# Kernel optimization log

Measured on AMD Instinct MI355X. Metric: run time of the kernel, lower is better.

The kernel has to match this reference:

```python
import jax, jax.numpy as jnp
import numpy as np


def setup_inputs() -> dict:
    key = jax.random.key(0)
    kL, kx = jax.random.split(key)
    N, D, K = 4096, 256, 8
    L = jax.random.normal(kL, (N, N), dtype=jnp.float32)
    x = jax.random.normal(kx, (N, D), dtype=jnp.float32)
    # Taylor-like decaying filter coefficients (fixed, non-trained in the original)
    coeffs = jnp.asarray([1.0, 0.9, 0.45, 0.15, 0.0375, 0.0075, 0.00125, 0.000179],
                         dtype=jnp.float32)
    return {"L": L, "x": x, "coeffs": coeffs}


def reference(L, x, coeffs):
    """filter = sum_i coeffs[i] * L^i ; out = filter @ x.

    Same math as torch.stack([c*L.matrix_power(i)]).sum(0) @ x, but the powers
    are built with a single running product instead of K independent
    matrix_power calls.
    """
    N = L.shape[0]
    K = coeffs.shape[0]
    P = jnp.eye(N, dtype=L.dtype)          # L^0
    filt = coeffs[0] * P
    for i in range(1, K):                   # small fixed polynomial order
        P = P @ L                            # L^i
        filt = filt + coeffs[i] * P
    return filt @ x                          # [N, D]
```

## Files before the change

kernel.cpp:

```cpp
#include <hip/hip_runtime.h>
#include <hip/hip_bf16.h>

#define NDIM 4096
#define DDIM 256
#define KORD 8

#define BM 128
#define BN 64
#define BK 32
#define SPLITK 4
#define KSLICE (NDIM / SPLITK)
#define NSTEP (KSLICE / BK)
#define ELEMS (NDIM * DDIM)

typedef __attribute__((ext_vector_type(8))) short bf16x8;
typedef __attribute__((ext_vector_type(4))) float f32x4;

__device__ __forceinline__ ushort f2bf(float v) {
    __hip_bfloat16 h = __float2bfloat16(v);
    return *reinterpret_cast<ushort*>(&h);
}
__device__ __forceinline__ float bf2f(ushort u) {
    __hip_bfloat16 h = *reinterpret_cast<__hip_bfloat16*>(&u);
    return __bfloat162float(h);
}
__device__ __forceinline__ void split2(float v, ushort& h, ushort& l) {
    h = f2bf(v);
    l = f2bf(v - bf2f(h));
}
__device__ __forceinline__ uint4 pack8(const ushort* s) {
    uint4 r;
    r.x = (uint)s[0] | ((uint)s[1] << 16);
    r.y = (uint)s[2] | ((uint)s[3] << 16);
    r.z = (uint)s[4] | ((uint)s[5] << 16);
    r.w = (uint)s[6] | ((uint)s[7] << 16);
    return r;
}

__global__ __launch_bounds__(256)
void split_L(const float* __restrict__ L, ushort* __restrict__ Lhi,
             ushort* __restrict__ Llo)
{
    const int e0 = (blockIdx.x * 256 + threadIdx.x) * 8;
    float4 a = *(const float4*)&L[e0];
    float4 b = *(const float4*)&L[e0 + 4];
    float v[8] = {a.x, a.y, a.z, a.w, b.x, b.y, b.z, b.w};
    ushort h[8], l[8];
#pragma unroll
    for (int j = 0; j < 8; ++j) split2(v[j], h[j], l[j]);
    *(uint4*)&Lhi[e0] = pack8(h);
    *(uint4*)&Llo[e0] = pack8(l);
}

__global__ __launch_bounds__(256)
void split_x(const float* __restrict__ x, const float* __restrict__ coeffs,
             ushort* __restrict__ yhiT, ushort* __restrict__ yloT)
{
    __shared__ float tile[64][65];
    const float c = coeffs[KORD - 1];
    const int m0 = blockIdx.x * 64, n0 = blockIdx.y * 64;
    const int t = threadIdx.x;
    const int ml = t >> 2, n4 = (t & 3) * 16;
#pragma unroll
    for (int j = 0; j < 4; ++j) {
        float4 v = *(const float4*)&x[(size_t)(m0 + ml) * DDIM + n0 + n4 + j * 4];
        tile[ml][n4 + j * 4 + 0] = c * v.x;
        tile[ml][n4 + j * 4 + 1] = c * v.y;
        tile[ml][n4 + j * 4 + 2] = c * v.z;
        tile[ml][n4 + j * 4 + 3] = c * v.w;
    }
    __syncthreads();
    const int nl = t >> 2, m16 = (t & 3) * 16;
    ushort h[16], l[16];
#pragma unroll
    for (int j = 0; j < 16; ++j) split2(tile[m16 + j][nl], h[j], l[j]);
    const size_t ob = (size_t)(n0 + nl) * NDIM + m0 + m16;
    *(uint4*)&yhiT[ob]     = pack8(h);
    *(uint4*)&yhiT[ob + 8] = pack8(h + 8);
    *(uint4*)&yloT[ob]     = pack8(l);
    *(uint4*)&yloT[ob + 8] = pack8(l + 8);
}

__global__ __launch_bounds__(256, 2)
void gemm_fused(const ushort* __restrict__ Lhi, const ushort* __restrict__ Llo,
                const ushort* __restrict__ yhiT, const ushort* __restrict__ yloT,
                float* __restrict__ P)
{
    __shared__ ushort lds[2][12288];

    const int bid  = blockIdx.x;
    const int xcd  = bid & 7;
    const int slot = bid >> 3;
    const int nt   = slot & 3;
    const int panel = xcd * 16 + (slot >> 2);
    const int mt = panel & 31;
    const int z  = panel >> 5;

    const int m0 = mt * BM, n0 = nt * BN;
    const int kb = z * KSLICE;

    const int t = threadIdx.x;
    const int lane = t & 63, wid = t >> 6;
    const int wr = wid >> 1, wc = wid & 1;

    const int srow = t >> 2;
    const int kswz = ((t & 3) ^ (srow & 3)) * 8;
    const ushort* aH0 = Lhi + (size_t)(m0 + srow) * NDIM + kb + kswz;
    const ushort* aH1 = aH0 + (size_t)64 * NDIM;
    const ushort* aL0 = Llo + (size_t)(m0 + srow) * NDIM + kb + kswz;
    const ushort* aL1 = aL0 + (size_t)64 * NDIM;
    const ushort* bH  = yhiT + (size_t)(n0 + srow) * NDIM + kb + kswz;
    const ushort* bL  = yloT + (size_t)(n0 + srow) * NDIM + kb + kswz;
    const int wb = wid * 512;

#define GLD(src, c, dstoff)                                                  \
    __builtin_amdgcn_global_load_lds(                                        \
        (const __attribute__((address_space(1))) uint*)(src),                \
        (__attribute__((address_space(3))) uint*)(&lds[c][dstoff]), 16, 0, 0)

    const int frow = lane & 15;
    const int fsw  = ((lane >> 4) ^ (frow & 3)) * 8;
    const int arB  = (wr * 64 + frow) * 32 + fsw;
    const int brB  = (wc * 32 + frow) * 32 + fsw;

    f32x4 acc[4][2];
#pragma unroll
    for (int i = 0; i < 4; ++i)
#pragma unroll
        for (int j = 0; j < 2; ++j) acc[i][j] = (f32x4){0.f, 0.f, 0.f, 0.f};

    {
        const int ko = 0;
        GLD(aH0 + ko, 0, wb);        GLD(aH1 + ko, 0, 2048 + wb);
        GLD(aL0 + ko, 0, 4096 + wb); GLD(aL1 + ko, 0, 6144 + wb);
        GLD(bH + ko, 0, 8192 + wb);  GLD(bL + ko, 0, 10240 + wb);
    }
    __syncthreads();

    int cur = 0;
    for (int step = 0; step < NSTEP; ++step) {
        if (step + 1 < NSTEP) {
            const int ko = (step + 1) * BK;
            const int c = cur ^ 1;
            GLD(aH0 + ko, c, wb);        GLD(aH1 + ko, c, 2048 + wb);
            GLD(aL0 + ko, c, 4096 + wb); GLD(aL1 + ko, c, 6144 + wb);
            GLD(bH + ko, c, 8192 + wb);  GLD(bL + ko, c, 10240 + wb);
        }

        bf16x8 ah[4], al[4], bh[2], blv[2];
#pragma unroll
        for (int i = 0; i < 4; ++i) {
            ah[i] = *(const bf16x8*)&lds[cur][arB + i * 512];
            al[i] = *(const bf16x8*)&lds[cur][arB + i * 512 + 4096];
        }
#pragma unroll
        for (int j = 0; j < 2; ++j) {
            bh[j]  = *(const bf16x8*)&lds[cur][8192 + brB + j * 512];
            blv[j] = *(const bf16x8*)&lds[cur][10240 + brB + j * 512];
        }
#pragma unroll
        for (int i = 0; i < 4; ++i)
#pragma unroll
            for (int j = 0; j < 2; ++j) {
                acc[i][j] = __builtin_amdgcn_mfma_f32_16x16x32_bf16(
                    ah[i], bh[j], acc[i][j], 0, 0, 0);
                acc[i][j] = __builtin_amdgcn_mfma_f32_16x16x32_bf16(
                    ah[i], blv[j], acc[i][j], 0, 0, 0);
                acc[i][j] = __builtin_amdgcn_mfma_f32_16x16x32_bf16(
                    al[i], bh[j], acc[i][j], 0, 0, 0);
            }
        __syncthreads();
        cur ^= 1;
    }
#undef GLD

    float* Pp = P + (size_t)z * ELEMS;
    const int crow = (lane >> 4) * 4;
    const int ccol = lane & 15;
#pragma unroll
    for (int i = 0; i < 4; ++i)
#pragma unroll
        for (int j = 0; j < 2; ++j)
#pragma unroll
            for (int r = 0; r < 4; ++r)
                Pp[(size_t)(m0 + wr * 64 + i * 16 + crow + r) * DDIM
                   + n0 + wc * 32 + j * 16 + ccol] = acc[i][j][r];
}

__global__ __launch_bounds__(256)
void combine(const float* __restrict__ P, const float* __restrict__ x,
             const float* __restrict__ coeffs, const int ci, const int last,
             ushort* __restrict__ yhiT, ushort* __restrict__ yloT,
             float* __restrict__ out)
{
    __shared__ float tile[64][65];
    const float c = coeffs[ci];
    const int m0 = blockIdx.x * 64, n0 = blockIdx.y * 64;
    const int t = threadIdx.x;
    const int ml = t >> 2, n4 = (t & 3) * 16;
    const size_t base = (size_t)(m0 + ml) * DDIM + n0 + n4;
    float acc[16];
#pragma unroll
    for (int j = 0; j < 4; ++j) {
        float4 v = *(const float4*)&x[base + j * 4];
        acc[j * 4 + 0] = c * v.x; acc[j * 4 + 1] = c * v.y;
        acc[j * 4 + 2] = c * v.z; acc[j * 4 + 3] = c * v.w;
    }
#pragma unroll
    for (int s = 0; s < SPLITK; ++s) {
        const float* Pp = P + (size_t)s * ELEMS;
#pragma unroll
        for (int j = 0; j < 4; ++j) {
            float4 v = *(const float4*)&Pp[base + j * 4];
            acc[j * 4 + 0] += v.x; acc[j * 4 + 1] += v.y;
            acc[j * 4 + 2] += v.z; acc[j * 4 + 3] += v.w;
        }
    }
    if (last) {
#pragma unroll
        for (int j = 0; j < 4; ++j) {
            float4 v;
            v.x = acc[j * 4 + 0]; v.y = acc[j * 4 + 1];
            v.z = acc[j * 4 + 2]; v.w = acc[j * 4 + 3];
            *(float4*)&out[base + j * 4] = v;
        }
        return;
    }
#pragma unroll
    for (int j = 0; j < 16; ++j) tile[ml][n4 + j] = acc[j];
    __syncthreads();
    const int nl = t >> 2, m16 = (t & 3) * 16;
    ushort h[16], l[16];
#pragma unroll
    for (int j = 0; j < 16; ++j) split2(tile[m16 + j][nl], h[j], l[j]);
    const size_t ob = (size_t)(n0 + nl) * NDIM + m0 + m16;
    *(uint4*)&yhiT[ob]     = pack8(h);
    *(uint4*)&yhiT[ob + 8] = pack8(h + 8);
    *(uint4*)&yloT[ob]     = pack8(l);
    *(uint4*)&yloT[ob + 8] = pack8(l + 8);
}

extern "C" void kernel_launch(void* const* d_in, const int* in_sizes, int n_in,
                              void* d_out, int out_size, void* d_ws, size_t ws_size,
                              hipStream_t stream)
{
    const float* L      = (const float*)d_in[0];
    const float* x      = (const float*)d_in[1];
    const float* coeffs = (const float*)d_in[2];
    float* out = (float*)d_out;

    char* w = (char*)d_ws;
    ushort* Lhi  = (ushort*)w;
    ushort* Llo  = (ushort*)(w + (size_t)NDIM * NDIM * 2);
    float*  Pp   = (float*)(w + (size_t)NDIM * NDIM * 4);
    ushort* yhiT = (ushort*)(w + (size_t)NDIM * NDIM * 4 + (size_t)SPLITK * ELEMS * 4);
    ushort* yloT = yhiT + (size_t)DDIM * NDIM;

    split_L<<<NDIM * NDIM / (256 * 8), 256, 0, stream>>>(L, Lhi, Llo);
    split_x<<<dim3(NDIM / 64, DDIM / 64), 256, 0, stream>>>(x, coeffs, yhiT, yloT);

    for (int i = KORD - 2; i >= 0; --i) {
        gemm_fused<<<SPLITK * 128, 256, 0, stream>>>(Lhi, Llo, yhiT, yloT, Pp);
        combine<<<dim3(NDIM / 64, DDIM / 64), 256, 0, stream>>>(
            Pp, x, coeffs, i, (i == 0) ? 1 : 0, yhiT, yloT, out);
    }
}
```

Baseline: 294.1 us.

## Widen GEMM tile to 128x128, deepen split-K and double-prefetch stages

The split-K GEMM tile grows from 128x64 to 128x128, so each block covers twice the output columns. This halves how many times the split L operand is re-read from memory. Split-K doubles to 8 to keep the same block count. The main loop now keeps two stages in flight, using explicit vmcnt waits and raw barriers in place of __syncthreads, and raises wave priority around the MFMA block. In exchange, the fp32 partial-sum buffer and the combine pass read twice as many partials, and the larger accumulator raises register pressure.

```diff
diff --git a/kernel.cpp b/kernel.cpp
--- a/kernel.cpp
+++ b/kernel.cpp
@@ -6,12 +6,14 @@
 #define KORD 8
 
 #define BM 128
-#define BN 64
+#define BN 128
 #define BK 32
-#define SPLITK 4
+#define SPLITK 8
 #define KSLICE (NDIM / SPLITK)
 #define NSTEP (KSLICE / BK)
 #define ELEMS (NDIM * DDIM)
+
+#define LBUF 16384
 
 typedef __attribute__((ext_vector_type(8))) short bf16x8;
 typedef __attribute__((ext_vector_type(4))) float f32x4;
@@ -86,15 +88,13 @@
                 const ushort* __restrict__ yhiT, const ushort* __restrict__ yloT,
                 float* __restrict__ P)
 {
-    __shared__ ushort lds[2][12288];
+    __shared__ ushort lds[2 * LBUF];
 
     const int bid  = blockIdx.x;
-    const int xcd  = bid & 7;
+    const int z    = bid & 7;
     const int slot = bid >> 3;
-    const int nt   = slot & 3;
-    const int panel = xcd * 16 + (slot >> 2);
-    const int mt = panel & 31;
-    const int z  = panel >> 5;
+    const int nt   = slot & 1;
+    const int mt   = slot >> 1;
 
     const int m0 = mt * BM, n0 = nt * BN;
     const int kb = z * KSLICE;
@@ -103,75 +103,90 @@
     const int lane = t & 63, wid = t >> 6;
     const int wr = wid >> 1, wc = wid & 1;
 
-    const int srow = t >> 2;
-    const int kswz = ((t & 3) ^ (srow & 3)) * 8;
-    const ushort* aH0 = Lhi + (size_t)(m0 + srow) * NDIM + kb + kswz;
-    const ushort* aH1 = aH0 + (size_t)64 * NDIM;
-    const ushort* aL0 = Llo + (size_t)(m0 + srow) * NDIM + kb + kswz;
-    const ushort* aL1 = aL0 + (size_t)64 * NDIM;
-    const ushort* bH  = yhiT + (size_t)(n0 + srow) * NDIM + kb + kswz;
-    const ushort* bL  = yloT + (size_t)(n0 + srow) * NDIM + kb + kswz;
+    const int rowS = t >> 2;
+    const int ksw  = ((t & 3) ^ (rowS & 3)) * 8;
+    const ushort* sAh = Lhi  + (size_t)(m0 + rowS) * NDIM + kb + ksw;
+    const ushort* sAl = Llo  + (size_t)(m0 + rowS) * NDIM + kb + ksw;
+    const ushort* sBh = yhiT + (size_t)(n0 + rowS) * NDIM + kb + ksw;
+    const ushort* sBl = yloT + (size_t)(n0 + rowS) * NDIM + kb + ksw;
+    const size_t R64 = (size_t)64 * NDIM;
     const int wb = wid * 512;
 
-#define GLD(src, c, dstoff)                                                  \
+#define GLD(src, dstoff)                                                     \
     __builtin_amdgcn_global_load_lds(                                        \
         (const __attribute__((address_space(1))) uint*)(src),                \
-        (__attribute__((address_space(3))) uint*)(&lds[c][dstoff]), 16, 0, 0)
+        (__attribute__((address_space(3))) uint*)(&lds[dstoff]), 16, 0, 0)
+
+#define STAGE(buf, ko)                                                       \
+    do {                                                                     \
+        const int _b = (buf) * LBUF;                                         \
+        GLD(sAh + (ko),        _b + wb);                                     \
+        GLD(sAh + (ko) + R64,  _b + 2048 + wb);                              \
+        GLD(sAl + (ko),        _b + 4096 + wb);                              \
+        GLD(sAl + (ko) + R64,  _b + 6144 + wb);                              \
+        GLD(sBh + (ko),        _b + 8192 + wb);                              \
+        GLD(sBh + (ko) + R64,  _b + 10240 + wb);                             \
+        GLD(sBl + (ko),        _b + 12288 + wb);                             \
+        GLD(sBl + (ko) + R64,  _b + 14336 + wb);                             \
+    } while (0)
 
     const int frow = lane & 15;
-    const int fsw  = ((lane >> 4) ^ (frow & 3)) * 8;
+    const int fsw  = (((lane >> 4) ^ (frow & 3))) * 8;
     const int arB  = (wr * 64 + frow) * 32 + fsw;
-    const int brB  = (wc * 32 + frow) * 32 + fsw;
-
-    f32x4 acc[4][2];
+    const int brB  = (wc * 64 + frow) * 32 + fsw;
+
+    f32x4 acc[4][4];
 #pragma unroll
     for (int i = 0; i < 4; ++i)
 #pragma unroll
-        for (int j = 0; j < 2; ++j) acc[i][j] = (f32x4){0.f, 0.f, 0.f, 0.f};
-
-    {
-        const int ko = 0;
-        GLD(aH0 + ko, 0, wb);        GLD(aH1 + ko, 0, 2048 + wb);
-        GLD(aL0 + ko, 0, 4096 + wb); GLD(aL1 + ko, 0, 6144 + wb);
-        GLD(bH + ko, 0, 8192 + wb);  GLD(bL + ko, 0, 10240 + wb);
-    }
-    __syncthreads();
-
-    int cur = 0;
+        for (int j = 0; j < 4; ++j) acc[i][j] = (f32x4){0.f, 0.f, 0.f, 0.f};
+
+    STAGE(0, 0);
+    STAGE(1, BK);
+
     for (int step = 0; step < NSTEP; ++step) {
-        if (step + 1 < NSTEP) {
-            const int ko = (step + 1) * BK;
-            const int c = cur ^ 1;
-            GLD(aH0 + ko, c, wb);        GLD(aH1 + ko, c, 2048 + wb);
-            GLD(aL0 + ko, c, 4096 + wb); GLD(aL1 + ko, c, 6144 + wb);
-            GLD(bH + ko, c, 8192 + wb);  GLD(bL + ko, c, 10240 + wb);
-        }
-
-        bf16x8 ah[4], al[4], bh[2], blv[2];
+        if (step + 1 < NSTEP)
+            asm volatile("s_waitcnt vmcnt(8)" ::: "memory");
+        else
+            asm volatile("s_waitcnt vmcnt(0)" ::: "memory");
+        __builtin_amdgcn_sched_barrier(0);
+        __builtin_amdgcn_s_barrier();
+        __builtin_amdgcn_sched_barrier(0);
+
+        const int b = (step & 1) * LBUF;
+        bf16x8 ah[4], al[4], bh[4], bl[4];
 #pragma unroll
         for (int i = 0; i < 4; ++i) {
-            ah[i] = *(const bf16x8*)&lds[cur][arB + i * 512];
-            al[i] = *(const bf16x8*)&lds[cur][arB + i * 512 + 4096];
-        }
-#pragma unroll
-        for (int j = 0; j < 2; ++j) {
-            bh[j]  = *(const bf16x8*)&lds[cur][8192 + brB + j * 512];
-            blv[j] = *(const bf16x8*)&lds[cur][10240 + brB + j * 512];
-        }
+            ah[i] = *(const bf16x8*)&lds[b + arB + i * 512];
+            al[i] = *(const bf16x8*)&lds[b + arB + i * 512 + 4096];
+        }
+#pragma unroll
+        for (int j = 0; j < 4; ++j) {
+            bh[j] = *(const bf16x8*)&lds[b + brB + j * 512 + 8192];
+            bl[j] = *(const bf16x8*)&lds[b + brB + j * 512 + 12288];
+        }
+        asm volatile("s_waitcnt lgkmcnt(0)" ::: "memory");
+        __builtin_amdgcn_sched_barrier(0);
+        __builtin_amdgcn_s_barrier();
+        __builtin_amdgcn_sched_barrier(0);
+
+        if (step + 2 < NSTEP) STAGE(step & 1, (step + 2) * BK);
+
+        __builtin_amdgcn_s_setprio(1);
 #pragma unroll
         for (int i = 0; i < 4; ++i)
 #pragma unroll
-            for (int j = 0; j < 2; ++j) {
+            for (int j = 0; j < 4; ++j) {
                 acc[i][j] = __builtin_amdgcn_mfma_f32_16x16x32_bf16(
                     ah[i], bh[j], acc[i][j], 0, 0, 0);
                 acc[i][j] = __builtin_amdgcn_mfma_f32_16x16x32_bf16(
-                    ah[i], blv[j], acc[i][j], 0, 0, 0);
+                    ah[i], bl[j], acc[i][j], 0, 0, 0);
                 acc[i][j] = __builtin_amdgcn_mfma_f32_16x16x32_bf16(
                     al[i], bh[j], acc[i][j], 0, 0, 0);
             }
-        __syncthreads();
-        cur ^= 1;
-    }
+        __builtin_amdgcn_s_setprio(0);
+    }
+#undef STAGE
 #undef GLD
 
     float* Pp = P + (size_t)z * ELEMS;
@@ -180,11 +195,11 @@
 #pragma unroll
     for (int i = 0; i < 4; ++i)
 #pragma unroll
-        for (int j = 0; j < 2; ++j)
+        for (int j = 0; j < 4; ++j)
 #pragma unroll
             for (int r = 0; r < 4; ++r)
                 Pp[(size_t)(m0 + wr * 64 + i * 16 + crow + r) * DDIM
-                   + n0 + wc * 32 + j * 16 + ccol] = acc[i][j][r];
+                   + n0 + wc * 64 + j * 16 + ccol] = acc[i][j][r];
 }
 
 __global__ __launch_bounds__(256)
@@ -260,7 +275,7 @@
     split_x<<<dim3(NDIM / 64, DDIM / 64), 256, 0, stream>>>(x, coeffs, yhiT, yloT);
 
     for (int i = KORD - 2; i >= 0; --i) {
-        gemm_fused<<<SPLITK * 128, 256, 0, stream>>>(Lhi, Llo, yhiT, yloT, Pp);
+        gemm_fused<<<SPLITK * 64, 256, 0, stream>>>(Lhi, Llo, yhiT, yloT, Pp);
         combine<<<dim3(NDIM / 64, DDIM / 64), 256, 0, stream>>>(
             Pp, x, coeffs, i, (i == 0) ? 1 : 0, yhiT, yloT, out);
     }
```

After: 320.7 us. +9.0%, slower.
